# Optimization experiments

Measured on AMD Instinct MI355X. Metric: run time of the kernel, lower is better.

Reference implementation:

```python
import jax, jax.numpy as jnp
import numpy as np

B, S, H, NH = 2, 2048, 768, 12
HD = H // NH  # 64
MAXPOS = 2048


def _rope_tables(max_pos, d):
    # bert4torch get_sinusoid_encoding_table: even cols sin, odd cols cos
    pos = np.arange(max_pos, dtype=np.float32)[:, None]
    div = np.exp(np.arange(0, d, 2, dtype=np.float32) * (-np.log(10000.0) / d))
    tab = np.zeros((max_pos, d), np.float32)
    tab[:, 0::2] = np.sin(pos * div)
    tab[:, 1::2] = np.cos(pos * div)
    cos = np.concatenate([tab[:, 1::2], tab[:, 1::2]], axis=1)  # [:,1::2].repeat(1,2)
    sin = np.concatenate([tab[:, 0::2], tab[:, 0::2]], axis=1)  # [:,0::2].repeat(1,2)
    return jnp.asarray(cos), jnp.asarray(sin)


def setup_inputs() -> dict:
    key = jax.random.key(0)
    ks = jax.random.split(key, 10)
    s = 0.02
    inp = {}
    inp["hidden_states"] = jax.random.normal(ks[0], (B, S, H), jnp.float32)
    inp["attention_mask"] = jnp.ones((B, 1, 1, S), jnp.float32)
    for i, n in enumerate(["q", "k", "v", "o"]):
        inp[f"W{n}"] = (jax.random.normal(ks[1 + i], (H, H), jnp.float32) * s)
        inp[f"b{n}"] = jnp.zeros((H,), jnp.float32)
    cos, sin = _rope_tables(MAXPOS, HD)
    inp["cos_position"] = cos
    inp["sin_position"] = sin
    return inp


def _apply_rope(qw, cos, sin):
    # Faithful to source: seq_len_dim defaults to 1, which on a
    # [B, heads, S, head_dim] tensor is the HEADS axis.
    L = qw.shape[1]
    qw2 = jnp.concatenate([-qw[..., 1::2], qw[..., 0::2]], axis=-1)
    return qw * cos[:L][None, :, None, :] + qw2 * sin[:L][None, :, None, :]


def reference(hidden_states, attention_mask, Wq, bq, Wk, bk, Wv, bv, Wo, bo,
              cos_position, sin_position):
    b, s, _ = hidden_states.shape

    def heads(x):  # [b,s,H] -> [b,NH,s,HD]
        return x.reshape(b, s, NH, HD).transpose(0, 2, 1, 3)

    q = heads(hidden_states @ Wq + bq)
    k = heads(hidden_states @ Wk + bk)
    v = heads(hidden_states @ Wv + bv)
    q = _apply_rope(q, cos_position, sin_position)
    k = _apply_rope(k, cos_position, sin_position)
    scores = jnp.einsum('bnid,bnjd->bnij', q, k) / jnp.sqrt(jnp.float32(HD))
    scores = scores + (1.0 - attention_mask) * (-10000.0)
    probs = jax.nn.softmax(scores, axis=-1)  # dropout is identity in eval
    ctx = jnp.einsum('bnij,bnjd->bnid', probs, v)
    ctx = ctx.transpose(0, 2, 1, 3).reshape(b, s, H)
    return ctx @ Wo + bo
```

## Files before the change

### kernel.cpp

```cpp
#include <hip/hip_runtime.h>

#define B 2
#define S 2048
#define H 768
#define NH 12
#define HD 64
#define BS (B * S)
#define LOG2E 1.4426950408889634f

typedef unsigned short u16;
typedef unsigned int u32;
typedef short short8 __attribute__((ext_vector_type(8)));
typedef float f32x4 __attribute__((ext_vector_type(4)));
typedef float f32x16 __attribute__((ext_vector_type(16)));

__device__ __forceinline__ u16 f2bf(float f) {
    union { float f; unsigned u; } c; c.f = f;
    unsigned u = c.u + 0x7FFFu + ((c.u >> 16) & 1u);
    return (u16)(u >> 16);
}
__device__ __forceinline__ float bf2f(u16 h) {
    union { unsigned u; float f; } c; c.u = ((unsigned)h) << 16;
    return c.f;
}
__device__ __forceinline__ f32x16 zero16() {
    f32x16 v;
    #pragma unroll
    for (int i = 0; i < 16; ++i) v[i] = 0.f;
    return v;
}
union pk4 { uint4 u; short8 s; };

__device__ __forceinline__ void g2l16(const u16* g, u16* l) {
    __builtin_amdgcn_global_load_lds(
        (const __attribute__((address_space(1))) void*)g,
        (__attribute__((address_space(3))) void*)l, 16, 0, 0);
}

__global__ __launch_bounds__(256) void prep_kernel(
    const float* __restrict__ hs,
    const float* __restrict__ Wq, const float* __restrict__ Wk,
    const float* __restrict__ Wv, const float* __restrict__ Wo,
    const float* __restrict__ bq, const float* __restrict__ bk,
    const float* __restrict__ cosp, const float* __restrict__ sinp,
    u16* __restrict__ hsb, u16* __restrict__ WTqkv, u16* __restrict__ WTo,
    float* __restrict__ bqk2)
{
    __shared__ float Lt[64 * 65];
    const int bid = blockIdx.x;
    const int t = threadIdx.x;

    if (bid >= 576) {
        size_t i = ((size_t)(bid - 576) * 256 + t) * 8;
        float4 a = *(const float4*)(hs + i);
        float4 b = *(const float4*)(hs + i + 4);
        short8 p;
        p[0] = (short)f2bf(a.x); p[1] = (short)f2bf(a.y);
        p[2] = (short)f2bf(a.z); p[3] = (short)f2bf(a.w);
        p[4] = (short)f2bf(b.x); p[5] = (short)f2bf(b.y);
        p[6] = (short)f2bf(b.z); p[7] = (short)f2bf(b.w);
        *(short8*)(hsb + i) = p;
        return;
    }

    const int z   = bid / 144;
    const int rem = bid - z * 144;
    const int k0 = (rem / 12) * 64, n0 = (rem % 12) * 64;
    const float* W = (z == 0) ? Wq : (z == 1) ? Wk : (z == 2) ? Wv : Wo;
    u16* D = (z == 3) ? WTo : (WTqkv + (size_t)z * H * H);
    const int head = n0 >> 6;
    const float scl = (z == 0) ? (0.125f * LOG2E) : 1.0f;

    if (z < 2 && rem / 12 == 0 && t < 64) {
        const float* bs = (z == 0) ? bq : bk;
        int d = t;
        int pd = (d < 32) ? (2 * d + 1) : (2 * (d - 32));
        float sv = ((d < 32) ? -1.f : 1.f) * sinp[head * HD + d];
        float cv = cosp[head * HD + d];
        bqk2[z * H + n0 + d] = scl * (cv * bs[n0 + d] + sv * bs[n0 + pd]);
    }

    #pragma unroll
    for (int u = 0; u < 4; ++u) {
        int f = t + u * 256;
        int r = f >> 4, c4 = (f & 15) * 4;
        float4 w = *(const float4*)(W + (size_t)(k0 + r) * H + n0 + c4);
        Lt[r * 65 + c4 + 0] = w.x; Lt[r * 65 + c4 + 1] = w.y;
        Lt[r * 65 + c4 + 2] = w.z; Lt[r * 65 + c4 + 3] = w.w;
    }
    __syncthreads();
    #pragma unroll
    for (int u = 0; u < 4; ++u) {
        int f = t + u * 256;
        int n = f >> 4, k4 = (f & 15) * 4;
        ushort4 p;
        if (z < 2) {
            int pn = (n < 32) ? (2 * n + 1) : (2 * (n - 32));
            float cv = scl * cosp[head * HD + n];
            float sv = scl * ((n < 32) ? -1.f : 1.f) * sinp[head * HD + n];
            p.x = f2bf(cv * Lt[(k4 + 0) * 65 + n] + sv * Lt[(k4 + 0) * 65 + pn]);
            p.y = f2bf(cv * Lt[(k4 + 1) * 65 + n] + sv * Lt[(k4 + 1) * 65 + pn]);
            p.z = f2bf(cv * Lt[(k4 + 2) * 65 + n] + sv * Lt[(k4 + 2) * 65 + pn]);
            p.w = f2bf(cv * Lt[(k4 + 3) * 65 + n] + sv * Lt[(k4 + 3) * 65 + pn]);
        } else {
            p.x = f2bf(Lt[(k4 + 0) * 65 + n]);
            p.y = f2bf(Lt[(k4 + 1) * 65 + n]);
            p.z = f2bf(Lt[(k4 + 2) * 65 + n]);
            p.w = f2bf(Lt[(k4 + 3) * 65 + n]);
        }
        *(ushort4*)(D + (size_t)(n0 + n) * H + k0 + k4) = p;
    }
}

__global__ __launch_bounds__(256) void gemm_qkv_kernel(
    const u16* __restrict__ A, const u16* __restrict__ BT,
    const float* __restrict__ bqk2, const float* __restrict__ bv,
    u16* __restrict__ Qb, u16* __restrict__ Kb, u16* __restrict__ VT)
{
    __shared__ alignas(16) u16 Abuf[2][128 * 64];
    __shared__ alignas(16) u16 Bbuf[2][128 * 64];

    const int tid  = threadIdx.x;
    const int w    = tid >> 6;
    const int lane = tid & 63;
    const int quad = lane >> 4;
    const int l15  = lane & 15;
    const int wm = (w & 1) * 64, wn = (w >> 1) * 64;
    const int m0 = (blockIdx.x & 31) * 128;
    const int n0 = (blockIdx.x >> 5) * 128;
    const int NK = H / 64;

    int srow[4], slc[4];
    #pragma unroll
    for (int u = 0; u < 4; ++u) {
        int s = u * 256 + tid;
        srow[u] = s >> 3;
        slc[u]  = (s & 7) ^ (srow[u] & 7);
    }

    #define QSTAGE(IT, NB)                                                    \
        _Pragma("unroll")                                                     \
        for (int u = 0; u < 4; ++u) {                                         \
            g2l16(A  + (size_t)(m0 + srow[u]) * H + (IT) * 64 + slc[u] * 8,   \
                  &Abuf[NB][(u * 256 + w * 64) * 8]);                         \
            g2l16(BT + (size_t)(n0 + srow[u]) * H + (IT) * 64 + slc[u] * 8,   \
                  &Bbuf[NB][(u * 256 + w * 64) * 8]);                         \
        }

    QSTAGE(0, 0)

    f32x4 acc[4][4];
    #pragma unroll
    for (int i = 0; i < 4; ++i)
        #pragma unroll
        for (int j = 0; j < 4; ++j) acc[i][j] = (f32x4){0.f, 0.f, 0.f, 0.f};

    for (int it = 0; it < NK; ++it) {
        const int cur = it & 1;
        __syncthreads();
        if (it + 1 < NK) { QSTAGE(it + 1, cur ^ 1) }

        const u16* Ac = Abuf[cur];
        const u16* Bc = Bbuf[cur];
        #pragma unroll
        for (int kc = 0; kc < 2; ++kc) {
            const int ch = kc * 4 + quad;
            short8 af[4], bf[4];
            #pragma unroll
            for (int mi = 0; mi < 4; ++mi) {
                int row = wm + mi * 16 + l15;
                af[mi] = *(const short8*)&Ac[row * 64 + (ch ^ (row & 7)) * 8];
            }
            #pragma unroll
            for (int ni = 0; ni < 4; ++ni) {
                int row = wn + ni * 16 + l15;
                bf[ni] = *(const short8*)&Bc[row * 64 + (ch ^ (row & 7)) * 8];
            }
            #pragma unroll
            for (int mi = 0; mi < 4; ++mi)
                #pragma unroll
                for (int ni = 0; ni < 4; ++ni)
                    acc[mi][ni] = __builtin_amdgcn_mfma_f32_16x16x32_bf16(
                        af[mi], bf[ni], acc[mi][ni], 0, 0, 0);
        }
    }
    #undef QSTAGE

    #pragma unroll
    for (int mi = 0; mi < 4; ++mi) {
        const int mbase = m0 + wm + mi * 16 + quad * 4;
        #pragma unroll
        for (int ni = 0; ni < 4; ++ni) {
            const int col = n0 + wn + ni * 16 + l15;
            const int which = col / H;
            const int c = col - which * H;
            const int h = c >> 6, d = c & 63;
            if (which == 2) {
                const float bias = bv[c];
                const int b_ = mbase >> 11, s = mbase & (S - 1);
                ushort4 pk;
                pk.x = f2bf(acc[mi][ni][0] + bias);
                pk.y = f2bf(acc[mi][ni][1] + bias);
                pk.z = f2bf(acc[mi][ni][2] + bias);
                pk.w = f2bf(acc[mi][ni][3] + bias);
                *(ushort4*)&VT[(((size_t)b_ * NH + h) * HD + d) * S + s] = pk;
            } else {
                u16* dst = (which == 0) ? Qb : Kb;
                const float bias = bqk2[which * H + c];
                #pragma unroll
                for (int r = 0; r < 4; ++r) {
                    int m = mbase + r;
                    int b_ = m >> 11, s = m & (S - 1);
                    dst[(((size_t)b_ * NH + h) * S + s) * HD + d] =
                        f2bf(acc[mi][ni][r] + bias);
                }
            }
        }
    }
}

__global__ __launch_bounds__(256) void gemm_out_kernel(
    const u16* __restrict__ A, const u16* __restrict__ BT,
    const float* __restrict__ bo, float* __restrict__ out)
{
    __shared__ alignas(16) u16 Abuf[2][128 * 64];
    __shared__ alignas(16) u16 Bbuf[2][64 * 64];

    const int tid  = threadIdx.x;
    const int w    = tid >> 6;
    const int lane = tid & 63;
    const int quad = lane >> 4;
    const int l15  = lane & 15;
    const int wm = (w & 1) * 64, wn = (w >> 1) * 32;
    const int m0 = (blockIdx.x & 31) * 128;
    const int n0 = (blockIdx.x >> 5) * 64;
    const int NK = H / 64;

    int srow[4], slc[4];
    #pragma unroll
    for (int u = 0; u < 4; ++u) {
        int s = u * 256 + tid;
        srow[u] = s >> 3;
        slc[u]  = (s & 7) ^ (srow[u] & 7);
    }

    #define OSTAGE(IT, NB)                                                    \
        _Pragma("unroll")                                                     \
        for (int u = 0; u < 4; ++u)                                           \
            g2l16(A + (size_t)(m0 + srow[u]) * H + (IT) * 64 + slc[u] * 8,    \
                  &Abuf[NB][(u * 256 + w * 64) * 8]);                         \
        _Pragma("unroll")                                                     \
        for (int u = 0; u < 2; ++u)                                           \
            g2l16(BT + (size_t)(n0 + srow[u]) * H + (IT) * 64 + slc[u] * 8,   \
                  &Bbuf[NB][(u * 256 + w * 64) * 8]);

    OSTAGE(0, 0)

    f32x4 acc[4][2];
    #pragma unroll
    for (int i = 0; i < 4; ++i)
        #pragma unroll
        for (int j = 0; j < 2; ++j) acc[i][j] = (f32x4){0.f, 0.f, 0.f, 0.f};

    for (int it = 0; it < NK; ++it) {
        const int cur = it & 1;
        __syncthreads();
        if (it + 1 < NK) { OSTAGE(it + 1, cur ^ 1) }

        const u16* Ac = Abuf[cur];
        const u16* Bc = Bbuf[cur];
        #pragma unroll
        for (int kc = 0; kc < 2; ++kc) {
            const int ch = kc * 4 + quad;
            short8 af[4], bf[2];
            #pragma unroll
            for (int mi = 0; mi < 4; ++mi) {
                int row = wm + mi * 16 + l15;
                af[mi] = *(const short8*)&Ac[row * 64 + (ch ^ (row & 7)) * 8];
            }
            #pragma unroll
            for (int ni = 0; ni < 2; ++ni) {
                int row = wn + ni * 16 + l15;
                bf[ni] = *(const short8*)&Bc[row * 64 + (ch ^ (row & 7)) * 8];
            }
            #pragma unroll
            for (int mi = 0; mi < 4; ++mi)
                #pragma unroll
                for (int ni = 0; ni < 2; ++ni)
                    acc[mi][ni] = __builtin_amdgcn_mfma_f32_16x16x32_bf16(
                        af[mi], bf[ni], acc[mi][ni], 0, 0, 0);
        }
    }
    #undef OSTAGE

    #pragma unroll
    for (int mi = 0; mi < 4; ++mi) {
        const int mbase = m0 + wm + mi * 16 + quad * 4;
        #pragma unroll
        for (int ni = 0; ni < 2; ++ni) {
            const int col = n0 + wn + ni * 16 + l15;
            const float bias = bo[col];
            #pragma unroll
            for (int r = 0; r < 4; ++r)
                out[(size_t)(mbase + r) * H + col] = acc[mi][ni][r] + bias;
        }
    }
}

__global__ __launch_bounds__(256, 3) void attn_mfma_kernel(
    const u16* __restrict__ Q, const u16* __restrict__ K,
    const u16* __restrict__ VT, const float* __restrict__ mask,
    u16* __restrict__ ctx)
{
    __shared__ alignas(16) u16 smem[26624];

    const int tid  = threadIdx.x;
    const int w    = tid >> 6;
    const int lane = tid & 63;
    const int l31  = lane & 31;
    const int h5   = lane >> 5;
    const int rh   = w & 1;
    const int kh   = w >> 1;
    const int bid = blockIdx.x;
    const int bn = bid % 24;
    const int q0 = (bid / 24) * 64;
    const int b = bn / NH, hh = bn % NH;
    const int NT = S / 64;

    short8 qa[4];
    {
        const u16* Qp = Q + ((size_t)bn * S + q0 + rh * 32 + l31) * HD + h5 * 8;
        #pragma unroll
        for (int kc = 0; kc < 4; ++kc)
            qa[kc] = *(const short8*)(Qp + kc * 16);
    }

    short8 oneb = {};
    if (h5 == 0) oneb[0] = (short)0x3F80;

    short8 onesa;
    #pragma unroll
    for (int i = 0; i < 8; ++i) onesa[i] = (short)0x3F80;

    const u16* Kg = K + (size_t)bn * S * HD;
    const u16* Vg = VT + (size_t)bn * HD * S;
    const float* mrow = mask + (size_t)b * S;
    u16* const mtl = smem + 24576;

    {
        const int i0 = tid * 8;
        float4 ma = *(const float4*)(mrow + i0);
        float4 mb = *(const float4*)(mrow + i0 + 4);
        const float c = -10000.0f * LOG2E;
        ushort4 p0, p1;
        p0.x = f2bf((1.0f - ma.x) * c); p0.y = f2bf((1.0f - ma.y) * c);
        p0.z = f2bf((1.0f - ma.z) * c); p0.w = f2bf((1.0f - ma.w) * c);
        p1.x = f2bf((1.0f - mb.x) * c); p1.y = f2bf((1.0f - mb.y) * c);
        p1.z = f2bf((1.0f - mb.z) * c); p1.w = f2bf((1.0f - mb.w) * c);
        *(ushort4*)(mtl + i0)     = p0;
        *(ushort4*)(mtl + i0 + 4) = p1;
    }

    int srow[2], slc[2];
    #pragma unroll
    for (int u = 0; u < 2; ++u) {
        int s = u * 256 + tid;
        srow[u] = s >> 3;
        slc[u]  = (s & 7) ^ (srow[u] & 7);
    }

    #define STAGE(JT, NB)                                                     \
        _Pragma("unroll")                                                     \
        for (int u = 0; u < 2; ++u) {                                         \
            g2l16(Kg + (size_t)((JT) * 64 + srow[u]) * HD + slc[u] * 8,       \
                  smem + (NB) * 8192 + (u * 256 + w * 64) * 8);               \
            g2l16(Vg + (size_t)srow[u] * S + (JT) * 64 + slc[u] * 8,          \
                  smem + (NB) * 8192 + 4096 + (u * 256 + w * 64) * 8);        \
        }

    asm volatile("s_waitcnt vmcnt(0) lgkmcnt(0)" ::: "memory");
    STAGE(0, 0)
    STAGE(1, 1)

    const f32x16 zc = zero16();
    f32x16 o0 = zero16(), o1 = zero16(), lac = zero16();
    const u32 psel = 0x07060302u;

    int cur = 0;
    for (int jt = 0; jt < NT; ++jt) {
        if (jt < NT - 1) asm volatile("s_waitcnt vmcnt(4)" ::: "memory");
        else             asm volatile("s_waitcnt vmcnt(0)" ::: "memory");
        __builtin_amdgcn_s_barrier();
        if (jt + 2 < NT) {
            const int nb = (cur >= 1) ? cur - 1 : cur + 2;
            STAGE(jt + 2, nb)
        }

        const u16* Kc = smem + cur * 8192;
        const u16* Vc = smem + cur * 8192 + 4096;

        const u16 mtv = mtl[jt * 64 + kh * 32 + l31];
        short8 mta = {};
        if (h5 == 0) mta[0] = (short)mtv;

        __builtin_amdgcn_s_setprio(1);
        f32x16 sc = __builtin_amdgcn_mfma_f32_32x32x16_bf16(
            mta, oneb, zc, 0, 0, 0);

        {
            const int krow = kh * 32 + l31;
            const int sw = krow & 7;
            #pragma unroll
            for (int kc = 0; kc < 4; ++kc) {
                const short8 kb =
                    *(const short8*)&Kc[krow * 64 + ((kc * 2 + h5) ^ sw) * 8];
                sc = __builtin_amdgcn_mfma_f32_32x32x16_bf16(kb, qa[kc], sc, 0, 0, 0);
            }
        }
        __builtin_amdgcn_s_setprio(0);

        short8 va[2][2];
        #pragma unroll
        for (int nt = 0; nt < 2; ++nt) {
            const int vrow = nt * 32 + l31;
            const int sw = vrow & 7;
            va[nt][0] = *(const short8*)&Vc[vrow * 64 + ((kh * 4 + h5) ^ sw) * 8];
            va[nt][1] = *(const short8*)&Vc[vrow * 64 + ((kh * 4 + 2 + h5) ^ sw) * 8];
        }

        u32 t[16];
        #pragma unroll
        for (int r = 0; r < 16; ++r) {
            union { float f; u32 u; } c;
            c.f = __builtin_amdgcn_exp2f(sc[r]);
            t[r] = c.u + 0x8000u;
        }
        u32 d[8];
        #pragma unroll
        for (int i = 0; i < 8; ++i)
            asm("v_perm_b32 %0, %1, %2, %3"
                : "=v"(d[i]) : "v"(t[2 * i + 1]), "v"(t[2 * i]), "s"(psel));

        u32 a0 = d[0], b0 = d[2];
        u32 a1 = d[1], b1 = d[3];
        u32 a2 = d[4], b2 = d[6];
        u32 a3 = d[5], b3 = d[7];
        asm("v_permlane32_swap_b32 %0, %1" : "+v"(a0), "+v"(b0));
        asm("v_permlane32_swap_b32 %0, %1" : "+v"(a1), "+v"(b1));
        asm("v_permlane32_swap_b32 %0, %1" : "+v"(a2), "+v"(b2));
        asm("v_permlane32_swap_b32 %0, %1" : "+v"(a3), "+v"(b3));

        pk4 f0, f1;
        f0.u = make_uint4(a0, a1, b0, b1);
        f1.u = make_uint4(a2, a3, b2, b3);

        __builtin_amdgcn_s_setprio(1);
        o0 = __builtin_amdgcn_mfma_f32_32x32x16_bf16(va[0][0], f0.s, o0, 0, 0, 0);
        o0 = __builtin_amdgcn_mfma_f32_32x32x16_bf16(va[0][1], f1.s, o0, 0, 0, 0);
        o1 = __builtin_amdgcn_mfma_f32_32x32x16_bf16(va[1][0], f0.s, o1, 0, 0, 0);
        o1 = __builtin_amdgcn_mfma_f32_32x32x16_bf16(va[1][1], f1.s, o1, 0, 0, 0);
        lac = __builtin_amdgcn_mfma_f32_32x32x16_bf16(onesa, f0.s, lac, 0, 0, 0);
        lac = __builtin_amdgcn_mfma_f32_32x32x16_bf16(onesa, f1.s, lac, 0, 0, 0);
        __builtin_amdgcn_s_setprio(0);

        cur = (cur == 2) ? 0 : cur + 1;
    }
    #undef STAGE

    float l_acc = lac[0];

    __syncthreads();
    float* cb = (float*)smem;
    float* lb = (float*)(smem + 8192);

    if (kh == 1) {
        #pragma unroll
        for (int r = 0; r < 16; ++r) {
            cb[r * 128 + rh * 64 + lane]        = o0[r];
            cb[(16 + r) * 128 + rh * 64 + lane] = o1[r];
        }
        if (h5 == 0) lb[rh * 32 + l31] = l_acc;
    }
    __syncthreads();
    if (kh == 0) {
        float lt = l_acc + lb[rh * 32 + l31];
        float inv = 1.0f / lt;
        const int s = q0 + rh * 32 + l31;
        u16* dst = ctx + ((size_t)b * S + s) * H + hh * 64;
        #pragma unroll
        for (int g = 0; g < 4; ++g) {
            ushort4 pk0, pk1;
            pk0.x = f2bf((o0[4 * g + 0] + cb[(4 * g + 0) * 128 + rh * 64 + lane]) * inv);
            pk0.y = f2bf((o0[4 * g + 1] + cb[(4 * g + 1) * 128 + rh * 64 + lane]) * inv);
            pk0.z = f2bf((o0[4 * g + 2] + cb[(4 * g + 2) * 128 + rh * 64 + lane]) * inv);
            pk0.w = f2bf((o0[4 * g + 3] + cb[(4 * g + 3) * 128 + rh * 64 + lane]) * inv);
            *(ushort4*)(dst + 8 * g + 4 * h5) = pk0;
            pk1.x = f2bf((o1[4 * g + 0] + cb[(16 + 4 * g + 0) * 128 + rh * 64 + lane]) * inv);
            pk1.y = f2bf((o1[4 * g + 1] + cb[(16 + 4 * g + 1) * 128 + rh * 64 + lane]) * inv);
            pk1.z = f2bf((o1[4 * g + 2] + cb[(16 + 4 * g + 2) * 128 + rh * 64 + lane]) * inv);
            pk1.w = f2bf((o1[4 * g + 3] + cb[(16 + 4 * g + 3) * 128 + rh * 64 + lane]) * inv);
            *(ushort4*)(dst + 32 + 8 * g + 4 * h5) = pk1;
        }
    }
}

extern "C" void kernel_launch(void* const* d_in, const int* in_sizes, int n_in,
                              void* d_out, int out_size, void* d_ws, size_t ws_size,
                              hipStream_t stream)
{
    const float* hs   = (const float*)d_in[0];
    const float* mask = (const float*)d_in[1];
    const float* Wq   = (const float*)d_in[2];
    const float* bq   = (const float*)d_in[3];
    const float* Wk   = (const float*)d_in[4];
    const float* bk   = (const float*)d_in[5];
    const float* Wv   = (const float*)d_in[6];
    const float* bv   = (const float*)d_in[7];
    const float* Wo   = (const float*)d_in[8];
    const float* bo   = (const float*)d_in[9];
    const float* cosp = (const float*)d_in[10];
    const float* sinp = (const float*)d_in[11];
    float* out = (float*)d_out;

    const size_t per = (size_t)B * NH * S * HD;
    u16* ws    = (u16*)d_ws;
    u16* hsb   = ws;
    u16* WTqkv = hsb + per;
    u16* WTo   = WTqkv + (size_t)3 * H * H;
    u16* Qb    = WTo + (size_t)H * H;
    u16* Kb    = Qb + per;
    u16* VT    = Kb + per;
    u16* ctxb  = VT + per;
    float* bqk2 = (float*)(ctxb + per);

    prep_kernel<<<576 + (BS * H) / 2048, 256, 0, stream>>>(
        hs, Wq, Wk, Wv, Wo, bq, bk, cosp, sinp, hsb, WTqkv, WTo, bqk2);

    gemm_qkv_kernel<<<(BS / 128) * (2304 / 128), 256, 0, stream>>>(
        hsb, WTqkv, bqk2, bv, Qb, Kb, VT);

    attn_mfma_kernel<<<(S / 64) * (B * NH), 256, 0, stream>>>(
        Qb, Kb, VT, mask, ctxb);

    gemm_out_kernel<<<(BS / 128) * (H / 64), 256, 0, stream>>>(
        ctxb, WTo, bo, out);
}
```

Before: 181.8 us.

## Software-pipeline attention QK with previous tile's softmax-PV and store Q transposed

The attention loop is restructured so the QK^T MFMAs for tile jt are issued before the softmax and PV work of tile jt-1, with three K/V stages prefetched and two barriers per iteration. This is meant to overlap the exp and permute VALU work with MFMA latency. Separately, the QKV GEMM now writes Q transposed with vectorized ushort4 stores, like V, instead of scattered scalar stores. The attention kernel then gathers Q with strided scalar loads, which makes the one-time Q load less efficient and adds register pressure from the live score tile.

```diff
diff --git a/kernel.cpp b/kernel.cpp
--- a/kernel.cpp
+++ b/kernel.cpp
@@ -115,7 +115,7 @@
 __global__ __launch_bounds__(256) void gemm_qkv_kernel(
     const u16* __restrict__ A, const u16* __restrict__ BT,
     const float* __restrict__ bqk2, const float* __restrict__ bv,
-    u16* __restrict__ Qb, u16* __restrict__ Kb, u16* __restrict__ VT)
+    u16* __restrict__ QTb, u16* __restrict__ Kb, u16* __restrict__ VT)
 {
     __shared__ alignas(16) u16 Abuf[2][128 * 64];
     __shared__ alignas(16) u16 Bbuf[2][128 * 64];
@@ -189,29 +189,29 @@
     #pragma unroll
     for (int mi = 0; mi < 4; ++mi) {
         const int mbase = m0 + wm + mi * 16 + quad * 4;
+        const int b_ = mbase >> 11, s = mbase & (S - 1);
         #pragma unroll
         for (int ni = 0; ni < 4; ++ni) {
             const int col = n0 + wn + ni * 16 + l15;
             const int which = col / H;
             const int c = col - which * H;
             const int h = c >> 6, d = c & 63;
-            if (which == 2) {
-                const float bias = bv[c];
-                const int b_ = mbase >> 11, s = mbase & (S - 1);
+            if (which != 1) {
+                const float bias = (which == 2) ? bv[c] : bqk2[c];
+                u16* dstT = (which == 2) ? VT : QTb;
                 ushort4 pk;
                 pk.x = f2bf(acc[mi][ni][0] + bias);
                 pk.y = f2bf(acc[mi][ni][1] + bias);
                 pk.z = f2bf(acc[mi][ni][2] + bias);
                 pk.w = f2bf(acc[mi][ni][3] + bias);
-                *(ushort4*)&VT[(((size_t)b_ * NH + h) * HD + d) * S + s] = pk;
+                *(ushort4*)&dstT[(((size_t)b_ * NH + h) * HD + d) * S + s] = pk;
             } else {
-                u16* dst = (which == 0) ? Qb : Kb;
-                const float bias = bqk2[which * H + c];
+                const float bias = bqk2[H + c];
                 #pragma unroll
                 for (int r = 0; r < 4; ++r) {
                     int m = mbase + r;
-                    int b_ = m >> 11, s = m & (S - 1);
-                    dst[(((size_t)b_ * NH + h) * S + s) * HD + d] =
+                    int bb = m >> 11, ss = m & (S - 1);
+                    Kb[(((size_t)bb * NH + h) * S + ss) * HD + d] =
                         f2bf(acc[mi][ni][r] + bias);
                 }
             }
@@ -308,7 +308,7 @@
 }
 
 __global__ __launch_bounds__(256, 3) void attn_mfma_kernel(
-    const u16* __restrict__ Q, const u16* __restrict__ K,
+    const u16* __restrict__ QT, const u16* __restrict__ K,
     const u16* __restrict__ VT, const float* __restrict__ mask,
     u16* __restrict__ ctx)
 {
@@ -329,10 +329,12 @@
 
     short8 qa[4];
     {
-        const u16* Qp = Q + ((size_t)bn * S + q0 + rh * 32 + l31) * HD + h5 * 8;
+        const u16* Qp = QT + (size_t)bn * HD * S + (q0 + rh * 32 + l31);
         #pragma unroll
         for (int kc = 0; kc < 4; ++kc)
-            qa[kc] = *(const short8*)(Qp + kc * 16);
+            #pragma unroll
+            for (int j = 0; j < 8; ++j)
+                qa[kc][j] = (short)Qp[(size_t)(kc * 16 + h5 * 8 + j) * S];
     }
 
     short8 oneb = {};
@@ -378,48 +380,30 @@
                   smem + (NB) * 8192 + 4096 + (u * 256 + w * 64) * 8);        \
         }
 
-    asm volatile("s_waitcnt vmcnt(0) lgkmcnt(0)" ::: "memory");
-    STAGE(0, 0)
-    STAGE(1, 1)
-
     const f32x16 zc = zero16();
     f32x16 o0 = zero16(), o1 = zero16(), lac = zero16();
     const u32 psel = 0x07060302u;
 
-    int cur = 0;
-    for (int jt = 0; jt < NT; ++jt) {
-        if (jt < NT - 1) asm volatile("s_waitcnt vmcnt(4)" ::: "memory");
-        else             asm volatile("s_waitcnt vmcnt(0)" ::: "memory");
-        __builtin_amdgcn_s_barrier();
-        if (jt + 2 < NT) {
-            const int nb = (cur >= 1) ? cur - 1 : cur + 2;
-            STAGE(jt + 2, nb)
-        }
-
-        const u16* Kc = smem + cur * 8192;
-        const u16* Vc = smem + cur * 8192 + 4096;
-
+    auto QK = [&](int jt, const u16* Kc) -> f32x16 {
         const u16 mtv = mtl[jt * 64 + kh * 32 + l31];
         short8 mta = {};
         if (h5 == 0) mta[0] = (short)mtv;
-
         __builtin_amdgcn_s_setprio(1);
         f32x16 sc = __builtin_amdgcn_mfma_f32_32x32x16_bf16(
             mta, oneb, zc, 0, 0, 0);
-
-        {
-            const int krow = kh * 32 + l31;
-            const int sw = krow & 7;
-            #pragma unroll
-            for (int kc = 0; kc < 4; ++kc) {
-                const short8 kb =
-                    *(const short8*)&Kc[krow * 64 + ((kc * 2 + h5) ^ sw) * 8];
-                sc = __builtin_amdgcn_mfma_f32_32x32x16_bf16(kb, qa[kc], sc, 0, 0, 0);
-            }
+        const int krow = kh * 32 + l31;
+        const int sw = krow & 7;
+        #pragma unroll
+        for (int kc = 0; kc < 4; ++kc) {
+            const short8 kb =
+                *(const short8*)&Kc[krow * 64 + ((kc * 2 + h5) ^ sw) * 8];
+            sc = __builtin_amdgcn_mfma_f32_32x32x16_bf16(kb, qa[kc], sc, 0, 0, 0);
         }
         __builtin_amdgcn_s_setprio(0);
-
-        short8 va[2][2];
+        return sc;
+    };
+
+    auto LDV = [&](const u16* Vc, short8 va[2][2]) {
         #pragma unroll
         for (int nt = 0; nt < 2; ++nt) {
             const int vrow = nt * 32 + l31;
@@ -427,7 +411,9 @@
             va[nt][0] = *(const short8*)&Vc[vrow * 64 + ((kh * 4 + h5) ^ sw) * 8];
             va[nt][1] = *(const short8*)&Vc[vrow * 64 + ((kh * 4 + 2 + h5) ^ sw) * 8];
         }
-
+    };
+
+    auto SMPV = [&](const f32x16& sc, const short8 va[2][2]) {
         u32 t[16];
         #pragma unroll
         for (int r = 0; r < 16; ++r) {
@@ -440,7 +426,6 @@
         for (int i = 0; i < 8; ++i)
             asm("v_perm_b32 %0, %1, %2, %3"
                 : "=v"(d[i]) : "v"(t[2 * i + 1]), "v"(t[2 * i]), "s"(psel));
-
         u32 a0 = d[0], b0 = d[2];
         u32 a1 = d[1], b1 = d[3];
         u32 a2 = d[4], b2 = d[6];
@@ -449,11 +434,9 @@
         asm("v_permlane32_swap_b32 %0, %1" : "+v"(a1), "+v"(b1));
         asm("v_permlane32_swap_b32 %0, %1" : "+v"(a2), "+v"(b2));
         asm("v_permlane32_swap_b32 %0, %1" : "+v"(a3), "+v"(b3));
-
         pk4 f0, f1;
         f0.u = make_uint4(a0, a1, b0, b1);
         f1.u = make_uint4(a2, a3, b2, b3);
-
         __builtin_amdgcn_s_setprio(1);
         o0 = __builtin_amdgcn_mfma_f32_32x32x16_bf16(va[0][0], f0.s, o0, 0, 0, 0);
         o0 = __builtin_amdgcn_mfma_f32_32x32x16_bf16(va[0][1], f1.s, o0, 0, 0, 0);
@@ -462,8 +445,37 @@
         lac = __builtin_amdgcn_mfma_f32_32x32x16_bf16(onesa, f0.s, lac, 0, 0, 0);
         lac = __builtin_amdgcn_mfma_f32_32x32x16_bf16(onesa, f1.s, lac, 0, 0, 0);
         __builtin_amdgcn_s_setprio(0);
-
-        cur = (cur == 2) ? 0 : cur + 1;
+    };
+
+    asm volatile("s_waitcnt vmcnt(0) lgkmcnt(0)" ::: "memory");
+    STAGE(0, 0)
+    STAGE(1, 1)
+    STAGE(2, 2)
+
+    asm volatile("s_waitcnt vmcnt(8)" ::: "memory");
+    __builtin_amdgcn_s_barrier();
+    f32x16 scp = QK(0, smem);
+
+    for (int jt = 1; jt < NT; ++jt) {
+        const int cb_ = jt % 3;
+        const int pb_ = (jt - 1) % 3;
+        short8 va[2][2];
+        LDV(smem + pb_ * 8192 + 4096, va);
+        asm volatile("s_waitcnt lgkmcnt(0)" ::: "memory");
+        __builtin_amdgcn_s_barrier();
+        if (jt <= NT - 3) { STAGE(jt + 2, pb_) }
+        if (jt <= NT - 3)      asm volatile("s_waitcnt vmcnt(8)" ::: "memory");
+        else if (jt == NT - 2) asm volatile("s_waitcnt vmcnt(4)" ::: "memory");
+        else                   asm volatile("s_waitcnt vmcnt(0)" ::: "memory");
+        __builtin_amdgcn_s_barrier();
+        f32x16 scn = QK(jt, smem + cb_ * 8192);
+        SMPV(scp, va);
+        scp = scn;
+    }
+    {
+        short8 va[2][2];
+        LDV(smem + ((NT - 1) % 3) * 8192 + 4096, va);
+        SMPV(scp, va);
     }
     #undef STAGE
 
@@ -527,8 +539,8 @@
     u16* hsb   = ws;
     u16* WTqkv = hsb + per;
     u16* WTo   = WTqkv + (size_t)3 * H * H;
-    u16* Qb    = WTo + (size_t)H * H;
-    u16* Kb    = Qb + per;
+    u16* QTb   = WTo + (size_t)H * H;
+    u16* Kb    = QTb + per;
     u16* VT    = Kb + per;
     u16* ctxb  = VT + per;
     float* bqk2 = (float*)(ctxb + per);
@@ -537,10 +549,10 @@
         hs, Wq, Wk, Wv, Wo, bq, bk, cosp, sinp, hsb, WTqkv, WTo, bqk2);
 
     gemm_qkv_kernel<<<(BS / 128) * (2304 / 128), 256, 0, stream>>>(
-        hsb, WTqkv, bqk2, bv, Qb, Kb, VT);
+        hsb, WTqkv, bqk2, bv, QTb, Kb, VT);
 
     attn_mfma_kernel<<<(S / 64) * (B * NH), 256, 0, stream>>>(
-        Qb, Kb, VT, mask, ctxb);
+        QTb, Kb, VT, mask, ctxb);
 
     gemm_out_kernel<<<(BS / 128) * (H / 64), 256, 0, stream>>>(
         ctxb, WTo, bo, out);
```

Result: no change. 182.5 us (+0.4%).
